# Optimization experiments

Measured on AMD Instinct MI355X. Metric: run time of the kernel, lower is better.

The kernel has to match this reference:

```python
import jax, jax.numpy as jnp
import numpy as np

S = 2048      # sequence length (prefill, start_idx=0)
D = 4096      # model dim
H = 32        # query heads
KVH = 8       # kv heads (GQA)
HD = D // H   # head dim = 128
ROPE_BASE = 500000.0  # llama3 rope theta
NEG = -1e9    # additive causal mask value (finite stand-in for -inf)


def setup_inputs() -> dict:
    key = jax.random.key(0)
    ks = jax.random.split(key, 5)
    scale = 1.0 / np.sqrt(D)
    x = jax.random.normal(ks[0], (S, D), jnp.float32)
    wq = jax.random.normal(ks[1], (D, D), jnp.float32) * scale
    wk = jax.random.normal(ks[2], (KVH * HD, D), jnp.float32) * scale
    wv = jax.random.normal(ks[3], (KVH * HD, D), jnp.float32) * scale
    wo = jax.random.normal(ks[4], (D, D), jnp.float32) * scale
    # RoPE tables, [S, HD//2]
    pos = jnp.arange(S, dtype=jnp.float32)
    inv_freq = 1.0 / (ROPE_BASE ** (jnp.arange(0, HD, 2, dtype=jnp.float32) / HD))
    ang = pos[:, None] * inv_freq[None, :]
    freqs_cos = jnp.cos(ang)
    freqs_sin = jnp.sin(ang)
    # additive causal mask [S, S]
    mask = jnp.where(jnp.tril(jnp.ones((S, S), bool)), 0.0, NEG).astype(jnp.float32)
    return dict(x=x, wq=wq, wk=wk, wv=wv, wo=wo, mask=mask,
                freqs_cos=freqs_cos, freqs_sin=freqs_sin)


def _rope(t, cos, sin):
    # t: [S, nh, hd]; cos/sin: [S, hd//2] -> interleaved even/odd rotation
    even = t[:, :, 0::2]
    odd = t[:, :, 1::2]
    c = cos[:, None, :]
    s = sin[:, None, :]
    re = even * c - odd * s
    im = even * s + odd * c
    return jnp.stack([re, im], axis=-1).reshape(t.shape)


def reference(x, wq, wk, wv, wo, mask, freqs_cos, freqs_sin):
    s, d = x.shape
    q = (x @ wq.T).reshape(s, H, HD)
    k = (x @ wk.T).reshape(s, KVH, HD)
    v = (x @ wv.T).reshape(s, KVH, HD)
    q = _rope(q, freqs_cos, freqs_sin)
    k = _rope(k, freqs_cos, freqs_sin)
    # KV-cache append at start_idx=0 then read back == identity (prefill)
    # GQA: repeat_interleave kv heads to match query heads
    k = jnp.repeat(k, H // KVH, axis=1)  # [s, H, HD]
    v = jnp.repeat(v, H // KVH, axis=1)
    logits = jnp.einsum('qhd,khd->hqk', q, k) * (1.0 / np.sqrt(HD)) + mask[None]
    p = jax.nn.softmax(logits, axis=-1)
    o = jnp.einsum('hqk,khd->qhd', p, v).reshape(s, d)
    return o @ wo.T
```

## Files before the change

kernel.cpp:

```cpp
#include <hip/hip_runtime.h>
#include <hip/hip_bf16.h>
#include <stdint.h>

#define S2   2048
#define DD   4096
#define NH   32
#define NKVH 8
#define HD2  128
#define QKVW 6144

typedef __bf16 bf16x8 __attribute__((ext_vector_type(8)));
typedef float  f32x4  __attribute__((ext_vector_type(4)));
typedef unsigned short u16x8 __attribute__((ext_vector_type(8)));
typedef unsigned short u16x4 __attribute__((ext_vector_type(4)));

__device__ __forceinline__ unsigned short f2b(float f) {
    unsigned int u = __builtin_bit_cast(unsigned int, f);
    unsigned int r = (u + 0x7FFFu + ((u >> 16) & 1u)) >> 16;
    return (unsigned short)r;
}
__device__ __forceinline__ float b2f(unsigned short h) {
    unsigned int u = ((unsigned int)h) << 16;
    return __builtin_bit_cast(float, u);
}
__device__ __forceinline__ unsigned cvt_pk_bf16(float a, float b) {
    unsigned r;
    asm("v_cvt_pk_bf16_f32 %0, %1, %2" : "=v"(r) : "v"(a), "v"(b));
    return r;
}

__device__ __forceinline__ void gload_lds16(const void* g, void* lds) {
    __builtin_amdgcn_global_load_lds(
        (const __attribute__((address_space(1))) void*)(uintptr_t)g,
        (__attribute__((address_space(3))) void*)(uint32_t)(uintptr_t)lds,
        16, 0, 0);
}

#define BAR() do { asm volatile("" ::: "memory"); \
                   __builtin_amdgcn_s_barrier();  \
                   asm volatile("" ::: "memory"); } while (0)
#define WAITV(n) asm volatile("s_waitcnt vmcnt(" #n ")" ::: "memory")

template<int N> __device__ __forceinline__ void waitv() {
    if      constexpr (N == 0)  WAITV(0);
    else if constexpr (N == 1)  WAITV(1);
    else if constexpr (N == 2)  WAITV(2);
    else if constexpr (N == 3)  WAITV(3);
    else if constexpr (N == 4)  WAITV(4);
    else if constexpr (N == 5)  WAITV(5);
    else if constexpr (N == 6)  WAITV(6);
    else if constexpr (N == 8)  WAITV(8);
}

__global__ void cvt_all(const float* __restrict__ x,  const float* __restrict__ wq,
                        const float* __restrict__ wk, const float* __restrict__ wv,
                        unsigned short* __restrict__ dst) {
    const long long NG = 8LL * 1024 * 1024;
    const long long stride = (long long)gridDim.x * blockDim.x;
    for (long long g = (long long)blockIdx.x * blockDim.x + threadIdx.x; g < NG; g += stride) {
        const float* src; long long off;
        if      (g < 2LL*1024*1024) { src = x;  off = g; }
        else if (g < 6LL*1024*1024) { src = wq; off = g - 2LL*1024*1024; }
        else if (g < 7LL*1024*1024) { src = wk; off = g - 6LL*1024*1024; }
        else                        { src = wv; off = g - 7LL*1024*1024; }
        f32x4 v = *reinterpret_cast<const f32x4*>(src + off * 4);
        u16x4 o;
        o[0] = f2b(v[0]); o[1] = f2b(v[1]); o[2] = f2b(v[2]); o[3] = f2b(v[3]);
        *reinterpret_cast<u16x4*>(dst + g * 4) = o;
    }
}

__global__ __launch_bounds__(512) void gemm_qkv(
    const unsigned short* __restrict__ A,
    const unsigned short* __restrict__ B0,
    const unsigned short* __restrict__ B1,
    const unsigned short* __restrict__ B2,
    unsigned short* __restrict__ C)
{
    constexpr int K = 4096, BK = 64, NT = K / BK;
    __shared__ unsigned short As[2][256 * 64];
    __shared__ unsigned short Bs[2][192 * 64];

    const int bm = blockIdx.y, bn = blockIdx.x;
    const int tid = threadIdx.x;
    const int w = tid >> 6, lane = tid & 63;
    const int wr = w >> 1, wc = w & 1;
    const int r16 = lane & 15, g4 = lane >> 4;

    const int bn0 = bn * 192;
    const unsigned short* Ap = A + (size_t)bm * 256 * K;

    const int lrow = lane >> 3;
    const int lchk = lane & 7;

    f32x4 acc[4][6] = {};
    bf16x8 af[4][2], b0[3][2], b1[3][2];

    auto browbase = [&](int rowg) -> const unsigned short* {
        if (rowg < 4096) return B0 + (size_t)rowg * K;
        if (rowg < 5120) return B1 + (size_t)(rowg - 4096) * K;
        return B2 + (size_t)(rowg - 5120) * K;
    };

    auto stageA = [&](int buf, int tt, int half) {
        #pragma unroll
        for (int i = 0; i < 2; ++i) {
            const int j = i * 8 + w;
            const int row0 = (j >> 2) * 64 + half * 32 + (j & 3) * 8;
            const int row = row0 + lrow;
            gload_lds16(Ap + (size_t)row * K + tt * BK + ((lchk ^ (row & 7)) * 8),
                        &As[buf][row0 * 64]);
        }
    };
    auto stageB = [&](int buf, int tt, int half) {
        #pragma unroll
        for (int i = 0; i < 2; ++i) {
            const int j = (i == 0) ? w : (8 + (w & 3));
            const int row0 = (j < 6) ? (half * 48 + j * 8)
                                     : (96 + half * 48 + (j - 6) * 8);
            const int row = row0 + lrow;
            const unsigned short* src = browbase(bn0 + row0) + (size_t)lrow * K;
            gload_lds16(src + tt * BK + ((lchk ^ (row & 7)) * 8),
                        &Bs[buf][row0 * 64]);
        }
    };
    auto readA = [&](int buf, int mh) {
        #pragma unroll
        for (int m = 0; m < 2; ++m)
            #pragma unroll
            for (int kk = 0; kk < 2; ++kk) {
                const int row = wr * 64 + mh * 32 + m * 16 + r16;
                af[mh * 2 + m][kk] = *reinterpret_cast<const bf16x8*>(
                    &As[buf][row * 64 + (((kk * 4 + g4) ^ (row & 7)) * 8)]);
            }
    };
    auto readB = [&](int buf, int nh, bf16x8 (&br)[3][2]) {
        #pragma unroll
        for (int n = 0; n < 3; ++n)
            #pragma unroll
            for (int kk = 0; kk < 2; ++kk) {
                const int row = wc * 96 + nh * 48 + n * 16 + r16;
                br[n][kk] = *reinterpret_cast<const bf16x8*>(
                    &Bs[buf][row * 64 + (((kk * 4 + g4) ^ (row & 7)) * 8)]);
            }
    };
    auto mma = [&](bf16x8 (&br)[3][2], int nh) {
        __builtin_amdgcn_s_setprio(1);
        #pragma unroll
        for (int m = 0; m < 4; ++m)
            #pragma unroll
            for (int n = 0; n < 3; ++n)
                #pragma unroll
                for (int kk = 0; kk < 2; ++kk)
                    acc[m][nh * 3 + n] = __builtin_amdgcn_mfma_f32_16x16x32_bf16(
                        af[m][kk], br[n][kk], acc[m][nh * 3 + n], 0, 0, 0);
        __builtin_amdgcn_s_setprio(0);
    };

    stageA(0, 0, 0); stageA(0, 0, 1); stageB(0, 0, 0); stageB(0, 0, 1);
    waitv<0>();
    BAR();

    for (int t = 0; t < NT - 1; ++t) {
        const int buf = t & 1;
        readA(buf, 0); readA(buf, 1); readB(buf, 0, b0);
        stageA(buf ^ 1, t + 1, 0); stageA(buf ^ 1, t + 1, 1); stageB(buf ^ 1, t + 1, 0);
        mma(b0, 0);
        waitv<6>();
        BAR();
        readB(buf, 1, b1);
        stageB(buf ^ 1, t + 1, 1);
        mma(b1, 1);
        waitv<2>();
        BAR();
    }
    {
        const int buf = (NT - 1) & 1;
        readA(buf, 0); readA(buf, 1); readB(buf, 0, b0);
        mma(b0, 0);
        waitv<0>();
        BAR();
        readB(buf, 1, b1);
        mma(b1, 1);
    }

    const size_t crow0 = (size_t)bm * 256 + wr * 64;
    const size_t ccol0 = (size_t)bn0 + wc * 96;
    #pragma unroll
    for (int m = 0; m < 4; ++m)
        #pragma unroll
        for (int n = 0; n < 6; ++n)
            #pragma unroll
            for (int r = 0; r < 4; ++r)
                C[(crow0 + m * 16 + g4 * 4 + r) * QKVW + ccol0 + n * 16 + r16] =
                    f2b(acc[m][n][r]);
}

__global__ __launch_bounds__(512) void gemm_out(
    const unsigned short* __restrict__ A,
    const unsigned short* __restrict__ B,
    float* __restrict__ C)
{
    constexpr int K = 4096, BK = 64, NT = K / BK;
    __shared__ unsigned short As[2][128 * 64];
    __shared__ unsigned short Bs[2][256 * 64];

    const int bm = blockIdx.y, bn = blockIdx.x;
    const int tid = threadIdx.x;
    const int w = tid >> 6, lane = tid & 63;
    const int wr = w >> 2, wc = w & 3;
    const int r16 = lane & 15, g4 = lane >> 4;

    const unsigned short* Ap = A + (size_t)bm * 128 * K;
    const unsigned short* Bp = B + (size_t)bn * 256 * K;

    const int lrow = lane >> 3;
    const int lchk = lane & 7;

    f32x4 acc[4][4] = {};
    bf16x8 af[4][2], b0[2][2], b1[2][2];

    auto stageA = [&](int buf, int tt, int half) {
        const int j = w;
        const int row0 = (j >> 2) * 64 + half * 32 + (j & 3) * 8;
        const int row = row0 + lrow;
        gload_lds16(Ap + (size_t)row * K + tt * BK + ((lchk ^ (row & 7)) * 8),
                    &As[buf][row0 * 64]);
    };
    auto stageB = [&](int buf, int tt, int half) {
        #pragma unroll
        for (int i = 0; i < 2; ++i) {
            const int j = i * 8 + w;
            const int row0 = (j >> 2) * 64 + half * 32 + (j & 3) * 8;
            const int row = row0 + lrow;
            gload_lds16(Bp + (size_t)row * K + tt * BK + ((lchk ^ (row & 7)) * 8),
                        &Bs[buf][row0 * 64]);
        }
    };
    auto readA = [&](int buf, int mh) {
        #pragma unroll
        for (int m = 0; m < 2; ++m)
            #pragma unroll
            for (int kk = 0; kk < 2; ++kk) {
                const int row = wr * 64 + mh * 32 + m * 16 + r16;
                af[mh * 2 + m][kk] = *reinterpret_cast<const bf16x8*>(
                    &As[buf][row * 64 + (((kk * 4 + g4) ^ (row & 7)) * 8)]);
            }
    };
    auto readB = [&](int buf, int nh, bf16x8 (&br)[2][2]) {
        #pragma unroll
        for (int n = 0; n < 2; ++n)
            #pragma unroll
            for (int kk = 0; kk < 2; ++kk) {
                const int row = wc * 64 + nh * 32 + n * 16 + r16;
                br[n][kk] = *reinterpret_cast<const bf16x8*>(
                    &Bs[buf][row * 64 + (((kk * 4 + g4) ^ (row & 7)) * 8)]);
            }
    };
    auto mma = [&](bf16x8 (&br)[2][2], int nh) {
        __builtin_amdgcn_s_setprio(1);
        #pragma unroll
        for (int m = 0; m < 4; ++m)
            #pragma unroll
            for (int n = 0; n < 2; ++n)
                #pragma unroll
                for (int kk = 0; kk < 2; ++kk)
                    acc[m][nh * 2 + n] = __builtin_amdgcn_mfma_f32_16x16x32_bf16(
                        af[m][kk], br[n][kk], acc[m][nh * 2 + n], 0, 0, 0);
        __builtin_amdgcn_s_setprio(0);
    };

    stageA(0, 0, 0); stageA(0, 0, 1); stageB(0, 0, 0); stageB(0, 0, 1);
    waitv<0>();
    BAR();

    for (int t = 0; t < NT - 1; ++t) {
        const int buf = t & 1;
        readA(buf, 0); readA(buf, 1); readB(buf, 0, b0);
        stageA(buf ^ 1, t + 1, 0); stageA(buf ^ 1, t + 1, 1); stageB(buf ^ 1, t + 1, 0);
        mma(b0, 0);
        waitv<4>();
        BAR();
        readB(buf, 1, b1);
        stageB(buf ^ 1, t + 1, 1);
        mma(b1, 1);
        waitv<2>();
        BAR();
    }
    {
        const int buf = (NT - 1) & 1;
        readA(buf, 0); readA(buf, 1); readB(buf, 0, b0);
        mma(b0, 0);
        waitv<0>();
        BAR();
        readB(buf, 1, b1);
        mma(b1, 1);
    }

    const size_t crow0 = (size_t)bm * 128 + wr * 64;
    const size_t ccol0 = (size_t)bn * 256 + wc * 64;
    #pragma unroll
    for (int m = 0; m < 4; ++m)
        #pragma unroll
        for (int n = 0; n < 4; ++n)
            #pragma unroll
            for (int r = 0; r < 4; ++r)
                C[(crow0 + m * 16 + g4 * 4 + r) * DD + ccol0 + n * 16 + r16] = acc[m][n][r];
}

__global__ __launch_bounds__(256) void rope_tv(unsigned short* __restrict__ qkv,
                                               const float* __restrict__ fc,
                                               const float* __restrict__ fs,
                                               unsigned short* __restrict__ Vt) {
    __shared__ unsigned short tile[64][72];
    const int bid = blockIdx.x;
    if (bid < 6144) {
        constexpr float QSCALE = 0.08838834764831845f * 1.4426950408889634f;
        const int g = (bid % 3) * 256 + threadIdx.x;
        if (g >= 640) return;
        const int s = bid / 3;
        const int col = g * 8;
        unsigned short* p = qkv + (size_t)s * QKVW + col;
        u16x8 v = *reinterpret_cast<const u16x8*>(p);
        const int i0 = (col & 127) >> 1;
        f32x4 c  = *reinterpret_cast<const f32x4*>(fc + s * 64 + i0);
        f32x4 sn = *reinterpret_cast<const f32x4*>(fs + s * 64 + i0);
        const float post = (col < DD) ? QSCALE : 1.0f;
        u16x8 o;
        #pragma unroll
        for (int j = 0; j < 4; ++j) {
            float e  = b2f(v[2*j]);
            float od = b2f(v[2*j+1]);
            o[2*j]   = f2b((e * c[j] - od * sn[j]) * post);
            o[2*j+1] = f2b((e * sn[j] + od * c[j]) * post);
        }
        *reinterpret_cast<u16x8*>(p) = o;
    } else {
        const int t = bid - 6144;
        const int d0g = (t & 15) * 64;
        const int s0  = (t >> 4) * 64;
        const int kvh = d0g >> 7, dl0 = d0g & 127;
        const int tid = threadIdx.x;
        #pragma unroll
        for (int p = 0; p < 2; ++p) {
            const int sgi = p * 256 + tid;
            const int srow = sgi >> 3, dseg = sgi & 7;
            u16x8 v = *reinterpret_cast<const u16x8*>(
                qkv + (size_t)(s0 + srow) * QKVW + 5120 + d0g + dseg * 8);
            #pragma unroll
            for (int j = 0; j < 8; ++j) tile[srow][dseg * 8 + j] = v[j];
        }
        __syncthreads();
        #pragma unroll
        for (int p = 0; p < 2; ++p) {
            const int sgi = p * 256 + tid;
            const int drow = sgi >> 3, sseg = sgi & 7;
            u16x8 v;
            #pragma unroll
            for (int j = 0; j < 8; ++j) v[j] = tile[sseg * 8 + j][drow];
            *reinterpret_cast<u16x8*>(
                Vt + (size_t)kvh * HD2 * S2 + (size_t)(dl0 + drow) * S2 + s0 + sseg * 8) = v;
        }
    }
}

__global__ __launch_bounds__(512) void attn_kernel(const unsigned short* __restrict__ Qkv,
                                                   const unsigned short* __restrict__ Vt,
                                                   unsigned short* __restrict__ O,
                                                   const float* __restrict__ wo_src,
                                                   unsigned short* __restrict__ wo_dst) {
    __shared__ unsigned short Klds[2][64 * 128];
    __shared__ unsigned short Vlds[2][128 * 64];
    __shared__ unsigned short Plds[8][2048];

    const int kvh = blockIdx.x;
    const int h   = kvh * 4 + (blockIdx.y & 3);
    const int p   = blockIdx.y >> 2;
    const int cB  = 8 + p, cS = 7 - p;
    const int w = threadIdx.x >> 6, lane = threadIdx.x & 63;
    const int tid = threadIdx.x;
    const int r16 = lane & 15, g4 = lane >> 4;

    const int myc = (w < 4) ? cB : cS;
    const int qw  = myc * 128 + (w & 3) * 32;
    const int ntB = 2 * cB + 2;

    const unsigned short* Kbase = Qkv + DD + kvh * HD2;
    const unsigned short* Vtb   = Vt + (size_t)kvh * HD2 * S2;
    char* pw = (char*)(&Plds[w][0]);

    const int blk = blockIdx.y * 8 + blockIdx.x;
    const f32x4* wo4 = (const f32x4*)wo_src;
    const int cb4 = blk * 16384 + tid;
    f32x4 cbuf[2];
    auto cvt_issue = [&](int k) {
        #pragma unroll
        for (int i = 0; i < 2; ++i)
            cbuf[i] = wo4[cb4 + k * 1024 + i * 512];
    };
    auto cvt_flush = [&](int k) {
        #pragma unroll
        for (int i = 0; i < 2; ++i) {
            u16x4 ov;
            ov[0] = f2b(cbuf[i][0]); ov[1] = f2b(cbuf[i][1]);
            ov[2] = f2b(cbuf[i][2]); ov[3] = f2b(cbuf[i][3]);
            *reinterpret_cast<u16x4*>(wo_dst + ((size_t)(cb4 + k * 1024 + i * 512)) * 4) = ov;
        }
    };

    const int krow_l = lane >> 4;
    const int kchunk = lane & 15;
    const int vd_l   = lane >> 3;
    const int vchunk = lane & 7;

    bf16x8 qf[2][4];
    #pragma unroll
    for (int m = 0; m < 2; ++m)
        #pragma unroll
        for (int f = 0; f < 4; ++f)
            qf[m][f] = *reinterpret_cast<const bf16x8*>(
                Qkv + (size_t)(qw + m * 16 + r16) * QKVW + h * HD2 + f * 32 + g4 * 8);

    f32x4 o[2][8] = {};
    float mr[2] = {-3e38f, -3e38f};
    float lr[2] = {0.f, 0.f};

    auto stage = [&](int buf, int kv0) {
        #pragma unroll
        for (int i = 0; i < 2; ++i) {
            const int seg = i * 8 + w;
            const int row = seg * 4 + krow_l;
            gload_lds16(Kbase + (size_t)(kv0 + row) * QKVW + ((kchunk ^ (row & 7)) * 8),
                        &Klds[buf][seg * 512]);
        }
        #pragma unroll
        for (int i = 0; i < 2; ++i) {
            const int seg = i * 8 + w;
            const int d = seg * 8 + vd_l;
            gload_lds16(Vtb + (size_t)d * S2 + kv0 + ((vchunk ^ (d & 7)) * 8),
                        &Vlds[buf][seg * 512]);
        }
    };

    stage(0, 0);
    WAITV(0);
    __syncthreads();
    cvt_issue(0);

    for (int t = 0; t < ntB; ++t) {
        if (t >= 1 && t <= 16) {
            cvt_flush(t - 1);
            if (t < 16) cvt_issue(t);
        }
        const int buf = t & 1;
        const int kv0 = t * 64;
        if (t + 1 < ntB) stage(buf ^ 1, (t + 1) * 64);

        if (kv0 <= qw + 31) {
            f32x4 sa[2][4] = {};
            #pragma unroll
            for (int kb = 0; kb < 4; ++kb) {
                bf16x8 kf[4];
                #pragma unroll
                for (int f = 0; f < 4; ++f)
                    kf[f] = *reinterpret_cast<const bf16x8*>(
                        &Klds[buf][(kb * 16 + r16) * 128 + (((f * 4 + g4) ^ (r16 & 7)) * 8)]);
                __builtin_amdgcn_s_setprio(1);
                #pragma unroll
                for (int m = 0; m < 2; ++m)
                    #pragma unroll
                    for (int f = 0; f < 4; ++f)
                        sa[m][kb] = __builtin_amdgcn_mfma_f32_16x16x32_bf16(
                            kf[f], qf[m][f], sa[m][kb], 0, 0, 0);
                __builtin_amdgcn_s_setprio(0);
            }
            const bool needmask = (kv0 + 63 > qw);
            float sv[2][4][4];
            #pragma unroll
            for (int m = 0; m < 2; ++m)
                #pragma unroll
                for (int kb = 0; kb < 4; ++kb)
                    #pragma unroll
                    for (int r = 0; r < 4; ++r) {
                        float xx = sa[m][kb][r];
                        if (needmask) {
                            const int kvg = kv0 + kb * 16 + g4 * 4 + r;
                            const int qg  = qw + m * 16 + r16;
                            xx = (kvg > qg) ? -3e38f : xx;
                        }
                        sv[m][kb][r] = xx;
                    }
            float rowm[2];
            #pragma unroll
            for (int m = 0; m < 2; ++m) {
                float a0 = fmaxf(fmaxf(sv[m][0][0], sv[m][0][1]), fmaxf(sv[m][0][2], sv[m][0][3]));
                float a1 = fmaxf(fmaxf(sv[m][1][0], sv[m][1][1]), fmaxf(sv[m][1][2], sv[m][1][3]));
                float a2 = fmaxf(fmaxf(sv[m][2][0], sv[m][2][1]), fmaxf(sv[m][2][2], sv[m][2][3]));
                float a3 = fmaxf(fmaxf(sv[m][3][0], sv[m][3][1]), fmaxf(sv[m][3][2], sv[m][3][3]));
                rowm[m] = fmaxf(fmaxf(a0, a1), fmaxf(a2, a3));
            }
            #pragma unroll
            for (int m = 0; m < 2; ++m) {
                rowm[m] = fmaxf(rowm[m], __shfl_xor(rowm[m], 16));
                rowm[m] = fmaxf(rowm[m], __shfl_xor(rowm[m], 32));
            }
            const float gmax = fmaxf(rowm[0] - mr[0], rowm[1] - mr[1]);
            if (!__all(gmax <= 11.5f)) {
                float corr[2];
                #pragma unroll
                for (int m = 0; m < 2; ++m) {
                    const float mn = fmaxf(mr[m], rowm[m]);
                    corr[m] = exp2f(mr[m] - mn);
                    mr[m] = mn;
                    lr[m] *= corr[m];
                }
                #pragma unroll
                for (int m = 0; m < 2; ++m)
                    #pragma unroll
                    for (int r = 0; r < 4; ++r) {
                        const float co = __shfl(corr[m], (lane & 48) | (g4 * 4 + r));
                        #pragma unroll
                        for (int n = 0; n < 8; ++n) o[m][n][r] *= co;
                    }
            }
            float rs[2] = {0.f, 0.f};
            #pragma unroll
            for (int m = 0; m < 2; ++m)
                #pragma unroll
                for (int kb = 0; kb < 4; ++kb)
                    #pragma unroll
                    for (int r = 0; r < 4; ++r) {
                        const float pp = exp2f(sv[m][kb][r] - mr[m]);
                        sv[m][kb][r] = pp;
                        rs[m] += pp;
                    }
            #pragma unroll
            for (int m = 0; m < 2; ++m) {
                rs[m] += __shfl_xor(rs[m], 16);
                rs[m] += __shfl_xor(rs[m], 32);
                lr[m] += rs[m];
            }
            #pragma unroll
            for (int m = 0; m < 2; ++m)
                #pragma unroll
                for (int kb = 0; kb < 4; ++kb) {
                    const unsigned w0 = cvt_pk_bf16(sv[m][kb][0], sv[m][kb][1]);
                    const unsigned w1 = cvt_pk_bf16(sv[m][kb][2], sv[m][kb][3]);
                    int wa = m * 2048 + ((kb * 2) + (g4 >> 1)) * 256 + r16 * 16 + (g4 & 1) * 8;
                    wa ^= (r16 >> 3) << 4;
                    *reinterpret_cast<unsigned long long*>(pw + wa) =
                        (unsigned long long)w0 | ((unsigned long long)w1 << 32);
                }
            asm volatile("s_waitcnt lgkmcnt(0)" ::: "memory");
            bf16x8 pa[2][2];
            #pragma unroll
            for (int m = 0; m < 2; ++m)
                #pragma unroll
                for (int kvs = 0; kvs < 2; ++kvs) {
                    int ra = m * 2048 + kvs * 1024 + lane * 16;
                    ra ^= (r16 >> 3) << 4;
                    pa[m][kvs] = *reinterpret_cast<const bf16x8*>(pw + ra);
                }
            #pragma unroll
            for (int kvs = 0; kvs < 2; ++kvs)
                #pragma unroll
                for (int n = 0; n < 8; ++n) {
                    const bf16x8 vb = *reinterpret_cast<const bf16x8*>(
                        &Vlds[buf][(n * 16 + r16) * 64 + (((kvs * 4 + g4) ^ (r16 & 7)) * 8)]);
                    __builtin_amdgcn_s_setprio(1);
                    #pragma unroll
                    for (int m = 0; m < 2; ++m)
                        o[m][n] = __builtin_amdgcn_mfma_f32_16x16x32_bf16(
                            pa[m][kvs], vb, o[m][n], 0, 0, 0);
                    __builtin_amdgcn_s_setprio(0);
                }
        }

        WAITV(0);
        __syncthreads();
    }

    float inv[2];
    #pragma unroll
    for (int m = 0; m < 2; ++m) inv[m] = 1.0f / lr[m];
    #pragma unroll
    for (int m = 0; m < 2; ++m)
        #pragma unroll
        for (int r = 0; r < 4; ++r) {
            const float iv = __shfl(inv[m], (lane & 48) | (g4 * 4 + r));
            #pragma unroll
            for (int n = 0; n < 8; ++n)
                O[(size_t)(qw + m * 16 + g4 * 4 + r) * DD + h * HD2 + n * 16 + r16] =
                    f2b(o[m][n][r] * iv);
        }
}

extern "C" void kernel_launch(void* const* d_in, const int* in_sizes, int n_in,
                              void* d_out, int out_size, void* d_ws, size_t ws_size,
                              hipStream_t stream) {
    (void)in_sizes; (void)n_in; (void)out_size; (void)ws_size;
    const float* x  = (const float*)d_in[0];
    const float* wq = (const float*)d_in[1];
    const float* wk = (const float*)d_in[2];
    const float* wv = (const float*)d_in[3];
    const float* wo = (const float*)d_in[4];
    const float* fc = (const float*)d_in[6];
    const float* fs = (const float*)d_in[7];
    float* out = (float*)d_out;

    unsigned short* ws = (unsigned short*)d_ws;
    const size_t M1 = 1024 * 1024;
    unsigned short* xb  = ws;
    unsigned short* wqb = ws + 8  * M1;
    unsigned short* wkb = ws + 24 * M1;
    unsigned short* wvb = ws + 28 * M1;
    unsigned short* wob = ws + 32 * M1;
    unsigned short* qkv = ws + 48 * M1;
    unsigned short* vt  = ws + 60 * M1;
    unsigned short* ob  = ws + 62 * M1;

    cvt_all<<<2048, 256, 0, stream>>>(x, wq, wk, wv, ws);
    gemm_qkv<<<dim3(32, 8), 512, 0, stream>>>(xb, wqb, wkb, wvb, qkv);
    rope_tv<<<6656, 256, 0, stream>>>(qkv, fc, fs, vt);
    attn_kernel<<<dim3(8, 32), 512, 0, stream>>>(qkv, vt, ob, wo, wob);
    gemm_out<<<dim3(16, 16), 512, 0, stream>>>(ob, wob, out);
}
```

Before: 282.0 us.

## Fuse RoPE, Q scaling and V transpose into QKV GEMM epilogue

The separate rope_tv kernel is removed. The QKV GEMM epilogue now applies RoPE to Q/K columns, using a lane shuffle to fetch each pair partner, and writes V directly in transposed layout. This saves one kernel launch and a full read and rewrite of the QKV buffer. Separately, the Wo fp32-to-bf16 conversion inside attention now batches four iterations of loads before flushing, so more loads are in flight at the cost of more registers. The epilogue stores are scalar and strided, and cos/sin are fetched per element, so the epilogue may get slower.

After: 290.7 us. 3.1% more time.

```diff
diff --git a/kernel.cpp b/kernel.cpp
--- a/kernel.cpp
+++ b/kernel.cpp
@@ -75,7 +75,10 @@
     const unsigned short* __restrict__ B0,
     const unsigned short* __restrict__ B1,
     const unsigned short* __restrict__ B2,
-    unsigned short* __restrict__ C)
+    unsigned short* __restrict__ C,
+    const float* __restrict__ fc,
+    const float* __restrict__ fs,
+    unsigned short* __restrict__ Vt)
 {
     constexpr int K = 4096, BK = 64, NT = K / BK;
     __shared__ unsigned short As[2][256 * 64];
@@ -184,16 +187,39 @@
         mma(b1, 1);
     }
 
-    const size_t crow0 = (size_t)bm * 256 + wr * 64;
-    const size_t ccol0 = (size_t)bn0 + wc * 96;
+    constexpr float QSCALE = 0.08838834764831845f * 1.4426950408889634f;
+    const int crow0 = bm * 256 + wr * 64;
+    const int ccol0 = bn0 + wc * 96;
     #pragma unroll
     for (int m = 0; m < 4; ++m)
         #pragma unroll
-        for (int n = 0; n < 6; ++n)
-            #pragma unroll
-            for (int r = 0; r < 4; ++r)
-                C[(crow0 + m * 16 + g4 * 4 + r) * QKVW + ccol0 + n * 16 + r16] =
-                    f2b(acc[m][n][r]);
+        for (int n = 0; n < 6; ++n) {
+            const int col = ccol0 + n * 16 + r16;
+            if (col < 5120) {
+                const int i0 = (col & 127) >> 1;
+                const float post = (col < 4096) ? QSCALE : 1.0f;
+                const bool ev = (col & 1) == 0;
+                #pragma unroll
+                for (int r = 0; r < 4; ++r) {
+                    const int row = crow0 + m * 16 + g4 * 4 + r;
+                    const float v  = acc[m][n][r];
+                    const float pv = __shfl_xor(v, 1);
+                    const float cc = fc[row * 64 + i0];
+                    const float ss = fs[row * 64 + i0];
+                    const float ov = ev ? (v * cc - pv * ss) : (pv * ss + v * cc);
+                    C[(size_t)row * QKVW + col] = f2b(ov * post);
+                }
+            } else {
+                const int dl  = col - 5120;
+                const int kvh = dl >> 7, d = dl & 127;
+                const int row0 = crow0 + m * 16 + g4 * 4;
+                u16x4 vv;
+                #pragma unroll
+                for (int r = 0; r < 4; ++r) vv[r] = f2b(acc[m][n][r]);
+                *reinterpret_cast<u16x4*>(
+                    Vt + (size_t)kvh * HD2 * S2 + (size_t)d * S2 + row0) = vv;
+            }
+        }
 }
 
 __global__ __launch_bounds__(512) void gemm_out(
@@ -308,62 +334,6 @@
                 C[(crow0 + m * 16 + g4 * 4 + r) * DD + ccol0 + n * 16 + r16] = acc[m][n][r];
 }
 
-__global__ __launch_bounds__(256) void rope_tv(unsigned short* __restrict__ qkv,
-                                               const float* __restrict__ fc,
-                                               const float* __restrict__ fs,
-                                               unsigned short* __restrict__ Vt) {
-    __shared__ unsigned short tile[64][72];
-    const int bid = blockIdx.x;
-    if (bid < 6144) {
-        constexpr float QSCALE = 0.08838834764831845f * 1.4426950408889634f;
-        const int g = (bid % 3) * 256 + threadIdx.x;
-        if (g >= 640) return;
-        const int s = bid / 3;
-        const int col = g * 8;
-        unsigned short* p = qkv + (size_t)s * QKVW + col;
-        u16x8 v = *reinterpret_cast<const u16x8*>(p);
-        const int i0 = (col & 127) >> 1;
-        f32x4 c  = *reinterpret_cast<const f32x4*>(fc + s * 64 + i0);
-        f32x4 sn = *reinterpret_cast<const f32x4*>(fs + s * 64 + i0);
-        const float post = (col < DD) ? QSCALE : 1.0f;
-        u16x8 o;
-        #pragma unroll
-        for (int j = 0; j < 4; ++j) {
-            float e  = b2f(v[2*j]);
-            float od = b2f(v[2*j+1]);
-            o[2*j]   = f2b((e * c[j] - od * sn[j]) * post);
-            o[2*j+1] = f2b((e * sn[j] + od * c[j]) * post);
-        }
-        *reinterpret_cast<u16x8*>(p) = o;
-    } else {
-        const int t = bid - 6144;
-        const int d0g = (t & 15) * 64;
-        const int s0  = (t >> 4) * 64;
-        const int kvh = d0g >> 7, dl0 = d0g & 127;
-        const int tid = threadIdx.x;
-        #pragma unroll
-        for (int p = 0; p < 2; ++p) {
-            const int sgi = p * 256 + tid;
-            const int srow = sgi >> 3, dseg = sgi & 7;
-            u16x8 v = *reinterpret_cast<const u16x8*>(
-                qkv + (size_t)(s0 + srow) * QKVW + 5120 + d0g + dseg * 8);
-            #pragma unroll
-            for (int j = 0; j < 8; ++j) tile[srow][dseg * 8 + j] = v[j];
-        }
-        __syncthreads();
-        #pragma unroll
-        for (int p = 0; p < 2; ++p) {
-            const int sgi = p * 256 + tid;
-            const int drow = sgi >> 3, sseg = sgi & 7;
-            u16x8 v;
-            #pragma unroll
-            for (int j = 0; j < 8; ++j) v[j] = tile[sseg * 8 + j][drow];
-            *reinterpret_cast<u16x8*>(
-                Vt + (size_t)kvh * HD2 * S2 + (size_t)(dl0 + drow) * S2 + s0 + sseg * 8) = v;
-        }
-    }
-}
-
 __global__ __launch_bounds__(512) void attn_kernel(const unsigned short* __restrict__ Qkv,
                                                    const unsigned short* __restrict__ Vt,
                                                    unsigned short* __restrict__ O,
@@ -392,20 +362,24 @@
     const int blk = blockIdx.y * 8 + blockIdx.x;
     const f32x4* wo4 = (const f32x4*)wo_src;
     const int cb4 = blk * 16384 + tid;
-    f32x4 cbuf[2];
+    f32x4 cbuf[8];
     auto cvt_issue = [&](int k) {
         #pragma unroll
         for (int i = 0; i < 2; ++i)
-            cbuf[i] = wo4[cb4 + k * 1024 + i * 512];
-    };
-    auto cvt_flush = [&](int k) {
-        #pragma unroll
-        for (int i = 0; i < 2; ++i) {
-            u16x4 ov;
-            ov[0] = f2b(cbuf[i][0]); ov[1] = f2b(cbuf[i][1]);
-            ov[2] = f2b(cbuf[i][2]); ov[3] = f2b(cbuf[i][3]);
-            *reinterpret_cast<u16x4*>(wo_dst + ((size_t)(cb4 + k * 1024 + i * 512)) * 4) = ov;
-        }
+            cbuf[(k & 3) * 2 + i] = wo4[cb4 + k * 1024 + i * 512];
+    };
+    auto cvt_flush4 = [&](int k0) {
+        #pragma unroll
+        for (int k = 0; k < 4; ++k)
+            #pragma unroll
+            for (int i = 0; i < 2; ++i) {
+                const f32x4 vsrc = cbuf[((k0 + k) & 3) * 2 + i];
+                u16x4 ov;
+                ov[0] = f2b(vsrc[0]); ov[1] = f2b(vsrc[1]);
+                ov[2] = f2b(vsrc[2]); ov[3] = f2b(vsrc[3]);
+                *reinterpret_cast<u16x4*>(
+                    wo_dst + ((size_t)(cb4 + (k0 + k) * 1024 + i * 512)) * 4) = ov;
+            }
     };
 
     const int krow_l = lane >> 4;
@@ -448,10 +422,8 @@
     cvt_issue(0);
 
     for (int t = 0; t < ntB; ++t) {
-        if (t >= 1 && t <= 16) {
-            cvt_flush(t - 1);
-            if (t < 16) cvt_issue(t);
-        }
+        if (t >= 4 && t <= 16 && (t & 3) == 0) cvt_flush4(t - 4);
+        if (t >= 1 && t < 16) cvt_issue(t);
         const int buf = t & 1;
         const int kv0 = t * 64;
         if (t + 1 < ntB) stage(buf ^ 1, (t + 1) * 64);
@@ -620,8 +592,7 @@
     unsigned short* ob  = ws + 62 * M1;
 
     cvt_all<<<2048, 256, 0, stream>>>(x, wq, wk, wv, ws);
-    gemm_qkv<<<dim3(32, 8), 512, 0, stream>>>(xb, wqb, wkb, wvb, qkv);
-    rope_tv<<<6656, 256, 0, stream>>>(qkv, fc, fs, vt);
+    gemm_qkv<<<dim3(32, 8), 512, 0, stream>>>(xb, wqb, wkb, wvb, qkv, fc, fs, vt);
     attn_kernel<<<dim3(8, 32), 512, 0, stream>>>(qkv, vt, ob, wo, wob);
     gemm_out<<<dim3(16, 16), 512, 0, stream>>>(ob, wob, out);
 }
```
